# Performance work log

Hardware: AMD Instinct MI355X
Metric: run time of the kernel (lower is better)

The kernel has to match this reference:

```python
import jax, jax.numpy as jnp
import numpy as np

N_NODES = 100000
N_EDGES = 3200000
N_GRAPHS = 128
IN_DIM = 4
HID = 64
BN_EPS = 1e-5


def setup_inputs() -> dict:
    key = jax.random.key(0)
    ks = jax.random.split(key, 24)
    x = jax.random.normal(ks[0], (N_NODES, IN_DIM), dtype=jnp.float32)
    edge_index = jax.random.randint(ks[1], (2, N_EDGES), 0, N_NODES, dtype=jnp.int32)
    batch_ids = jnp.sort(jax.random.randint(ks[2], (N_NODES,), 0, N_GRAPHS, dtype=jnp.int32))

    def lin(k, out_d, in_d):
        s = 1.0 / np.sqrt(in_d)
        return jax.random.uniform(k, (out_d, in_d), jnp.float32, -s, s)

    inp = {
        'x': x, 'edge_index': edge_index, 'batch_ids': batch_ids,
        # SAGEConv i: out = lin_l(mean_neighbors) + lin_r(x_self); bias lives in lin_l
        'w1l': lin(ks[3], HID, IN_DIM), 'b1': jnp.zeros((HID,), jnp.float32), 'w1r': lin(ks[4], HID, IN_DIM),
        'bn1_g': jnp.ones((HID,), jnp.float32), 'bn1_b': jnp.zeros((HID,), jnp.float32),
        'w2l': lin(ks[5], HID, HID), 'b2': jnp.zeros((HID,), jnp.float32), 'w2r': lin(ks[6], HID, HID),
        'bn2_g': jnp.ones((HID,), jnp.float32), 'bn2_b': jnp.zeros((HID,), jnp.float32),
        'w3l': lin(ks[7], HID, HID), 'b3': jnp.zeros((HID,), jnp.float32), 'w3r': lin(ks[8], HID, HID),
        'bn3_g': jnp.ones((HID,), jnp.float32), 'bn3_b': jnp.zeros((HID,), jnp.float32),
        'fc1_w': lin(ks[9], 64, HID), 'fc1_b': jnp.zeros((64,), jnp.float32),
        'fc2_w': lin(ks[10], 2, 64), 'fc2_b': jnp.zeros((2,), jnp.float32),
    }
    return inp


def _sage(x, src, dst, deg_inv, wl, bl, wr):
    # mean-aggregate neighbor messages (source -> target), then two small GEMMs
    msum = jax.ops.segment_sum(x[src], dst, num_segments=N_NODES)  # [N, d]
    agg = msum * deg_inv[:, None]
    return agg @ wl.T + bl + x @ wr.T


def _bn(x, g, b):
    # BatchNorm1d in training mode: batch stats over node dim, biased variance
    m = jnp.mean(x, axis=0)
    v = jnp.mean((x - m) ** 2, axis=0)
    return (x - m) * jax.lax.rsqrt(v + BN_EPS) * g + b


def reference(x, edge_index, batch_ids,
              w1l, b1, w1r, bn1_g, bn1_b,
              w2l, b2, w2r, bn2_g, bn2_b,
              w3l, b3, w3r, bn3_g, bn3_b,
              fc1_w, fc1_b, fc2_w, fc2_b):
    src, dst = edge_index[0], edge_index[1]
    deg = jax.ops.segment_sum(jnp.ones((src.shape[0],), x.dtype), dst, num_segments=N_NODES)
    deg_inv = 1.0 / jnp.maximum(deg, 1.0)

    h = jax.nn.relu(_bn(_sage(x, src, dst, deg_inv, w1l, b1, w1r), bn1_g, bn1_b))
    h = jax.nn.relu(_bn(_sage(h, src, dst, deg_inv, w2l, b2, w2r), bn2_g, bn2_b))
    h = jax.nn.relu(_bn(_sage(h, src, dst, deg_inv, w3l, b3, w3r), bn3_g, bn3_b))

    # global_mean_pool over graphs
    gsum = jax.ops.segment_sum(h, batch_ids, num_segments=N_GRAPHS)
    gcnt = jax.ops.segment_sum(jnp.ones((h.shape[0],), h.dtype), batch_ids, num_segments=N_GRAPHS)
    pooled = gsum / jnp.maximum(gcnt, 1.0)[:, None]

    # MLP head (dropout = identity at inference)
    hid = jax.nn.relu(pooled @ fc1_w.T + fc1_b)
    return hid @ fc2_w.T + fc2_b
```

## Files before the change

kernel.cpp:

```cpp
#include <hip/hip_runtime.h>
#include <hip/hip_fp16.h>

#define NN 100000
#define NE 3200000
#define NG 128
#define BN_EPS 1e-5f

#define NBUK 782
#define BSHIFT 7
#define BCAP 6144

#define GRID_SG 1024
#define PBMAX 2048

typedef _Float16 h2v __attribute__((ext_vector_type(2)));

__global__ void __launch_bounds__(512) k_scatter(
    const int* __restrict__ src, const int* __restrict__ dst,
    int* __restrict__ slab_cursor, unsigned int* __restrict__ slab, int E) {
    __shared__ int hist[NBUK + 2];
    __shared__ int cbase[NBUK + 2];
    int tid = threadIdx.x;
    int eBeg = blockIdx.x * 6250;
    int eEnd = min(eBeg + 6250, E);

    for (int t = tid; t < NBUK; t += 512) hist[t] = 0;
    __syncthreads();
    for (int e = eBeg + tid; e < eEnd; e += 512) {
        int b = dst[e] >> BSHIFT;
        atomicAdd(&hist[b], 1);
    }
    __syncthreads();
    for (int t = tid; t < NBUK; t += 512) {
        int c = hist[t];
        cbase[t] = (c > 0) ? atomicAdd(&slab_cursor[t], c) : 0;
    }
    __syncthreads();
    for (int t = tid; t < NBUK; t += 512) hist[t] = 0;
    __syncthreads();
    for (int e = eBeg + tid; e < eEnd; e += 512) {
        int d = dst[e];
        int b = d >> BSHIFT;
        int r = atomicAdd(&hist[b], 1);
        int pos = cbase[b] + r;
        if (pos < BCAP) slab[(size_t)b * BCAP + pos] = ((unsigned)src[e] << BSHIFT) | (unsigned)(d & 127);
    }
}

__global__ void k_bucket_scan(const int* __restrict__ slab_cursor,
                              int* __restrict__ bucket_base, int* __restrict__ row_ptr) {
    __shared__ int sm[1024];
    int t = threadIdx.x;
    int c = (t < NBUK) ? min(slab_cursor[t], BCAP) : 0;
    sm[t] = c;
    __syncthreads();
    for (int off = 1; off < 1024; off <<= 1) {
        int add = (t >= off) ? sm[t - off] : 0;
        __syncthreads();
        sm[t] += add;
        __syncthreads();
    }
    if (t < NBUK) {
        bucket_base[t] = sm[t] - c;
        if (t == NBUK - 1) row_ptr[NN] = sm[t];
    }
}

__global__ void __launch_bounds__(512) k_bucket_csr(
    const unsigned int* __restrict__ slab, const int* __restrict__ slab_cursor,
    const int* __restrict__ bucket_base, int* __restrict__ row_ptr,
    float* __restrict__ deg_inv, int* __restrict__ csr_src,
    const float* __restrict__ x, const float* __restrict__ w1l,
    const float* __restrict__ b1, const float* __restrict__ w1r,
    float* __restrict__ h_pre, float* __restrict__ part) {
    __shared__ int lds_csr[BCAP];
    __shared__ int sdeg[128];
    __shared__ int sscan[128];
    __shared__ int slcur[128];
    __shared__ float swl[256], swr[256], sb1[64];
    __shared__ float ssum[64], ssq[64];
    int tid = threadIdx.x;
    int b = blockIdx.x;
    int lo = b << BSHIFT;
    int cnt = min(slab_cursor[b], BCAP);
    const unsigned int* sl = slab + (size_t)b * BCAP;

    if (tid < 256) { swl[tid] = w1l[tid]; swr[tid] = w1r[tid]; }
    if (tid < 64)  { sb1[tid] = b1[tid]; ssum[tid] = 0.f; ssq[tid] = 0.f; }
    if (tid < 128) sdeg[tid] = 0;
    __syncthreads();
    for (int k = tid; k < cnt; k += 512) {
        atomicAdd(&sdeg[sl[k] & 127], 1);
    }
    __syncthreads();
    int v = (tid < 128) ? sdeg[tid] : 0;
    if (tid < 128) sscan[tid] = v;
    __syncthreads();
    for (int off = 1; off < 128; off <<= 1) {
        int add = 0;
        if (tid < 128 && tid >= off) add = sscan[tid - off];
        __syncthreads();
        if (tid < 128) sscan[tid] += add;
        __syncthreads();
    }
    int base = bucket_base[b];
    if (tid < 128) {
        int excl = sscan[tid] - v;
        int n = lo + tid;
        if (n < NN) {
            row_ptr[n] = base + excl;
            deg_inv[n] = 1.0f / fmaxf((float)v, 1.0f);
        }
        slcur[tid] = excl;
    }
    __syncthreads();
    for (int k = tid; k < cnt; k += 512) {
        unsigned int p = sl[k];
        int pos = atomicAdd(&slcur[p & 127], 1);
        lds_csr[pos] = (int)(p >> BSHIFT);
    }
    __syncthreads();
    for (int k = tid; k < cnt; k += 512) csr_src[base + k] = lds_csr[k];

    int i = tid >> 2, c = tid & 3;
    int n = lo + i;
    bool valid = (n < NN);
    int dhi = sscan[i];
    int dlo = dhi - sdeg[i];
    const float4* x4 = (const float4*)x;
    float4 acc = make_float4(0.f, 0.f, 0.f, 0.f);
    for (int k = dlo + c; k < dhi; k += 4) {
        int s = lds_csr[k];
        float4 xv = x4[s];
        acc.x += xv.x; acc.y += xv.y; acc.z += xv.z; acc.w += xv.w;
    }
#pragma unroll
    for (int m = 1; m <= 2; m <<= 1) {
        acc.x += __shfl_xor(acc.x, m);
        acc.y += __shfl_xor(acc.y, m);
        acc.z += __shfl_xor(acc.z, m);
        acc.w += __shfl_xor(acc.w, m);
    }
    float dv = 1.0f / fmaxf((float)sdeg[i], 1.0f);
    float ax = acc.x * dv, ay = acc.y * dv, az = acc.z * dv, aw = acc.w * dv;
    float4 xs = valid ? x4[n] : make_float4(0.f, 0.f, 0.f, 0.f);

#pragma unroll
    for (int m4 = 0; m4 < 4; m4++) {
        float4 o = make_float4(0.f, 0.f, 0.f, 0.f);
        float* op = &o.x;
        if (valid) {
#pragma unroll
            for (int t = 0; t < 4; t++) {
                int j = c * 16 + m4 * 4 + t;
                float s = sb1[j];
                s += ax * swl[j * 4 + 0] + ay * swl[j * 4 + 1] + az * swl[j * 4 + 2] + aw * swl[j * 4 + 3];
                s += xs.x * swr[j * 4 + 0] + xs.y * swr[j * 4 + 1] + xs.z * swr[j * 4 + 2] + xs.w * swr[j * 4 + 3];
                op[t] = s;
            }
            ((float4*)h_pre)[(size_t)n * 16 + c * 4 + m4] = o;
        }
        float4 q = make_float4(o.x * o.x, o.y * o.y, o.z * o.z, o.w * o.w);
#pragma unroll
        for (int m = 4; m <= 32; m <<= 1) {
            o.x += __shfl_xor(o.x, m); o.y += __shfl_xor(o.y, m);
            o.z += __shfl_xor(o.z, m); o.w += __shfl_xor(o.w, m);
            q.x += __shfl_xor(q.x, m); q.y += __shfl_xor(q.y, m);
            q.z += __shfl_xor(q.z, m); q.w += __shfl_xor(q.w, m);
        }
        if ((tid & 63) < 4) {
            int jb = c * 16 + m4 * 4;
            atomicAdd(&ssum[jb + 0], o.x); atomicAdd(&ssum[jb + 1], o.y);
            atomicAdd(&ssum[jb + 2], o.z); atomicAdd(&ssum[jb + 3], o.w);
            atomicAdd(&ssq[jb + 0], q.x);  atomicAdd(&ssq[jb + 1], q.y);
            atomicAdd(&ssq[jb + 2], q.z);  atomicAdd(&ssq[jb + 3], q.w);
        }
    }
    __syncthreads();
    if (tid < 64) {
        part[(2 * tid) * PBMAX + blockIdx.x]     = ssum[tid];
        part[(2 * tid + 1) * PBMAX + blockIdx.x] = ssq[tid];
    }
}

__global__ void __launch_bounds__(512, 8) k_sage(
    const __half* __restrict__ h_in, const int* __restrict__ row_ptr,
    const int* __restrict__ csr_src, const float* __restrict__ deg_inv,
    const float* __restrict__ wl, const float* __restrict__ bl,
    const float* __restrict__ wr, float* __restrict__ h_pre,
    float* __restrict__ part) {
    __shared__ h2v wl2s[32][68];
    __shared__ h2v wr2s[32][68];
    __shared__ h2v tAh[32][36];
    __shared__ h2v tXh[32][36];
    __shared__ float ssum[64], ssq[64];
    int tid = threadIdx.x;
    for (int idx = tid; idx < 2048; idx += 512) {
        int j = idx & 63, kk = idx >> 6;
        float2 l = ((const float2*)wl)[j * 32 + kk];
        float2 r = ((const float2*)wr)[j * 32 + kk];
        wl2s[kk][j] = h2v{(_Float16)l.x, (_Float16)l.y};
        wr2s[kk][j] = h2v{(_Float16)r.x, (_Float16)r.y};
    }
    if (tid < 64) { ssum[tid] = 0.f; ssq[tid] = 0.f; }
    __syncthreads();

    int g = tid & 15, ni = tid >> 4;
    const uint2* tbl = (const uint2*)h_in;
    const int ntiles = NN / 32;

    for (int tile = blockIdx.x; tile < ntiles; tile += gridDim.x) {
        int n = tile * 32 + ni;
        float ax = 0.f, ay = 0.f, az = 0.f, aw = 0.f;
        int r0 = row_ptr[n], r1 = row_ptr[n + 1];
        int e = r0;
        for (; e + 8 <= r1; e += 8) {
            int s0 = csr_src[e],     s1 = csr_src[e + 1], s2 = csr_src[e + 2], s3 = csr_src[e + 3];
            int s4 = csr_src[e + 4], s5 = csr_src[e + 5], s6 = csr_src[e + 6], s7 = csr_src[e + 7];
            uint2 v0 = tbl[(size_t)s0 * 16 + g];
            uint2 v1 = tbl[(size_t)s1 * 16 + g];
            uint2 v2 = tbl[(size_t)s2 * 16 + g];
            uint2 v3 = tbl[(size_t)s3 * 16 + g];
            uint2 v4 = tbl[(size_t)s4 * 16 + g];
            uint2 v5 = tbl[(size_t)s5 * 16 + g];
            uint2 v6 = tbl[(size_t)s6 * 16 + g];
            uint2 v7 = tbl[(size_t)s7 * 16 + g];
            float2 f;
            f = __half22float2(*(__half2*)&v0.x); ax += f.x; ay += f.y;
            f = __half22float2(*(__half2*)&v0.y); az += f.x; aw += f.y;
            f = __half22float2(*(__half2*)&v1.x); ax += f.x; ay += f.y;
            f = __half22float2(*(__half2*)&v1.y); az += f.x; aw += f.y;
            f = __half22float2(*(__half2*)&v2.x); ax += f.x; ay += f.y;
            f = __half22float2(*(__half2*)&v2.y); az += f.x; aw += f.y;
            f = __half22float2(*(__half2*)&v3.x); ax += f.x; ay += f.y;
            f = __half22float2(*(__half2*)&v3.y); az += f.x; aw += f.y;
            f = __half22float2(*(__half2*)&v4.x); ax += f.x; ay += f.y;
            f = __half22float2(*(__half2*)&v4.y); az += f.x; aw += f.y;
            f = __half22float2(*(__half2*)&v5.x); ax += f.x; ay += f.y;
            f = __half22float2(*(__half2*)&v5.y); az += f.x; aw += f.y;
            f = __half22float2(*(__half2*)&v6.x); ax += f.x; ay += f.y;
            f = __half22float2(*(__half2*)&v6.y); az += f.x; aw += f.y;
            f = __half22float2(*(__half2*)&v7.x); ax += f.x; ay += f.y;
            f = __half22float2(*(__half2*)&v7.y); az += f.x; aw += f.y;
        }
        for (; e < r1; ++e) {
            int s = csr_src[e];
            uint2 v = tbl[(size_t)s * 16 + g];
            float2 f;
            f = __half22float2(*(__half2*)&v.x); ax += f.x; ay += f.y;
            f = __half22float2(*(__half2*)&v.y); az += f.x; aw += f.y;
        }
        float di = deg_inv[n];
        uint2 rs = tbl[(size_t)n * 16 + g];
        ax *= di; ay *= di; az *= di; aw *= di;
        tAh[ni][2 * g]     = h2v{(_Float16)ax, (_Float16)ay};
        tAh[ni][2 * g + 1] = h2v{(_Float16)az, (_Float16)aw};
        *(uint2*)&tXh[ni][2 * g] = rs;
        __syncthreads();

        float4 o = ((const float4*)bl)[g];
#pragma unroll 4
        for (int kk = 0; kk < 32; kk++) {
            h2v a2 = tAh[ni][kk];
            h2v x2 = tXh[ni][kk];
            h2v l0 = wl2s[kk][4 * g + 0], l1 = wl2s[kk][4 * g + 1];
            h2v l2 = wl2s[kk][4 * g + 2], l3 = wl2s[kk][4 * g + 3];
            h2v r0v = wr2s[kk][4 * g + 0], r1v = wr2s[kk][4 * g + 1];
            h2v r2v = wr2s[kk][4 * g + 2], r3v = wr2s[kk][4 * g + 3];
#if __has_builtin(__builtin_amdgcn_fdot2)
            o.x = __builtin_amdgcn_fdot2(a2, l0, o.x, false);
            o.y = __builtin_amdgcn_fdot2(a2, l1, o.y, false);
            o.z = __builtin_amdgcn_fdot2(a2, l2, o.z, false);
            o.w = __builtin_amdgcn_fdot2(a2, l3, o.w, false);
            o.x = __builtin_amdgcn_fdot2(x2, r0v, o.x, false);
            o.y = __builtin_amdgcn_fdot2(x2, r1v, o.y, false);
            o.z = __builtin_amdgcn_fdot2(x2, r2v, o.z, false);
            o.w = __builtin_amdgcn_fdot2(x2, r3v, o.w, false);
#else
            float b0 = (float)a2.x, b1 = (float)a2.y, x0 = (float)x2.x, x1 = (float)x2.y;
            o.x += b0 * (float)l0.x + b1 * (float)l0.y + x0 * (float)r0v.x + x1 * (float)r0v.y;
            o.y += b0 * (float)l1.x + b1 * (float)l1.y + x0 * (float)r1v.x + x1 * (float)r1v.y;
            o.z += b0 * (float)l2.x + b1 * (float)l2.y + x0 * (float)r2v.x + x1 * (float)r2v.y;
            o.w += b0 * (float)l3.x + b1 * (float)l3.y + x0 * (float)r3v.x + x1 * (float)r3v.y;
#endif
        }
        ((float4*)h_pre)[(size_t)n * 16 + g] = o;

        float4 qv = make_float4(o.x * o.x, o.y * o.y, o.z * o.z, o.w * o.w);
#pragma unroll
        for (int m = 16; m <= 32; m <<= 1) {
            o.x += __shfl_xor(o.x, m); o.y += __shfl_xor(o.y, m);
            o.z += __shfl_xor(o.z, m); o.w += __shfl_xor(o.w, m);
            qv.x += __shfl_xor(qv.x, m); qv.y += __shfl_xor(qv.y, m);
            qv.z += __shfl_xor(qv.z, m); qv.w += __shfl_xor(qv.w, m);
        }
        if ((tid & 48) == 0) {
            atomicAdd(&ssum[4 * g + 0], o.x); atomicAdd(&ssum[4 * g + 1], o.y);
            atomicAdd(&ssum[4 * g + 2], o.z); atomicAdd(&ssum[4 * g + 3], o.w);
            atomicAdd(&ssq[4 * g + 0], qv.x);  atomicAdd(&ssq[4 * g + 1], qv.y);
            atomicAdd(&ssq[4 * g + 2], qv.z);  atomicAdd(&ssq[4 * g + 3], qv.w);
        }
        __syncthreads();
    }
    if (tid < 64) {
        part[(2 * tid) * PBMAX + blockIdx.x]     = ssum[tid];
        part[(2 * tid + 1) * PBMAX + blockIdx.x] = ssq[tid];
    }
}

__global__ void k_reduce_sb(const float* __restrict__ part, int PB,
                            const float* __restrict__ gamma, const float* __restrict__ beta,
                            float* __restrict__ sbv, int N) {
    int c = blockIdx.x;
    float s = 0.f, q = 0.f;
    for (int b = threadIdx.x; b < PB; b += 256) {
        s += part[(2 * c) * PBMAX + b];
        q += part[(2 * c + 1) * PBMAX + b];
    }
    __shared__ float rs[256], rq[256];
    rs[threadIdx.x] = s;
    rq[threadIdx.x] = q;
    __syncthreads();
    for (int off = 128; off > 0; off >>= 1) {
        if (threadIdx.x < off) {
            rs[threadIdx.x] += rs[threadIdx.x + off];
            rq[threadIdx.x] += rq[threadIdx.x + off];
        }
        __syncthreads();
    }
    if (threadIdx.x == 0) {
        float m = rs[0] / (float)N;
        float var = rq[0] / (float)N - m * m;
        float sc = gamma[c] * rsqrtf(var + BN_EPS);
        sbv[c]      = sc;
        sbv[64 + c] = beta[c] - m * sc;
    }
}

__global__ void k_bnrelu_h(const float* __restrict__ h_pre, const float* __restrict__ sbv,
                           __half* __restrict__ h, int N) {
    __shared__ float s_sc[64], s_bi[64];
    if (threadIdx.x < 64) {
        s_sc[threadIdx.x] = sbv[threadIdx.x];
        s_bi[threadIdx.x] = sbv[64 + threadIdx.x];
    }
    __syncthreads();
    int total = N * 16;
    for (int i = blockIdx.x * blockDim.x + threadIdx.x; i < total; i += gridDim.x * blockDim.x) {
        float4 v = ((const float4*)h_pre)[i];
        int c4 = (i & 15) * 4;
        v.x = fmaxf(v.x * s_sc[c4 + 0] + s_bi[c4 + 0], 0.f);
        v.y = fmaxf(v.y * s_sc[c4 + 1] + s_bi[c4 + 1], 0.f);
        v.z = fmaxf(v.z * s_sc[c4 + 2] + s_bi[c4 + 2], 0.f);
        v.w = fmaxf(v.w * s_sc[c4 + 3] + s_bi[c4 + 3], 0.f);
        __half2 p0 = __floats2half2_rn(v.x, v.y);
        __half2 p1 = __floats2half2_rn(v.z, v.w);
        uint2 o;
        o.x = *(unsigned int*)&p0;
        o.y = *(unsigned int*)&p1;
        ((uint2*)h)[i] = o;
    }
}

__global__ void k_poolhead(const __half* __restrict__ h, const int* __restrict__ batch,
                           const float* __restrict__ fc1w, const float* __restrict__ fc1b,
                           const float* __restrict__ fc2w, const float* __restrict__ fc2b,
                           float* __restrict__ out, int N) {
    int gph = blockIdx.x;
    int lo = 0, hi = N;
    while (lo < hi) { int mid = (lo + hi) >> 1; if (batch[mid] < gph) lo = mid + 1; else hi = mid; }
    int start = lo;
    hi = N;
    while (lo < hi) { int mid = (lo + hi) >> 1; if (batch[mid] < gph + 1) lo = mid + 1; else hi = mid; }
    int end = lo;

    int c = threadIdx.x & 63, w = threadIdx.x >> 6;
    float s = 0.f;
    for (int r = start + w; r < end; r += 4) s += __half2float(h[(size_t)r * 64 + c]);
    __shared__ float sm[256];
    __shared__ float pl[64], hid[64];
    sm[threadIdx.x] = s;
    __syncthreads();
    if (threadIdx.x < 64) {
        float t = sm[c] + sm[64 + c] + sm[128 + c] + sm[192 + c];
        pl[c] = t / fmaxf((float)(end - start), 1.0f);
    }
    __syncthreads();
    if (threadIdx.x < 64) {
        int j = threadIdx.x;
        float v = fc1b[j];
        for (int k = 0; k < 64; k++) v += pl[k] * fc1w[j * 64 + k];
        hid[j] = fmaxf(v, 0.f);
    }
    __syncthreads();
    if (threadIdx.x < 2) {
        int j = threadIdx.x;
        float o = fc2b[j];
        for (int k = 0; k < 64; k++) o += hid[k] * fc2w[j * 64 + k];
        out[gph * 2 + j] = o;
    }
}

extern "C" void kernel_launch(void* const* d_in, const int* in_sizes, int n_in,
                              void* d_out, int out_size, void* d_ws, size_t ws_size,
                              hipStream_t stream) {
    const float* x    = (const float*)d_in[0];
    const int* ei     = (const int*)d_in[1];
    const int* batch  = (const int*)d_in[2];
    const float* w1l  = (const float*)d_in[3];
    const float* b1   = (const float*)d_in[4];
    const float* w1r  = (const float*)d_in[5];
    const float* bn1g = (const float*)d_in[6];
    const float* bn1b = (const float*)d_in[7];
    const float* w2l  = (const float*)d_in[8];
    const float* b2   = (const float*)d_in[9];
    const float* w2r  = (const float*)d_in[10];
    const float* bn2g = (const float*)d_in[11];
    const float* bn2b = (const float*)d_in[12];
    const float* w3l  = (const float*)d_in[13];
    const float* b3   = (const float*)d_in[14];
    const float* w3r  = (const float*)d_in[15];
    const float* bn3g = (const float*)d_in[16];
    const float* bn3b = (const float*)d_in[17];
    const float* fc1w = (const float*)d_in[18];
    const float* fc1b = (const float*)d_in[19];
    const float* fc2w = (const float*)d_in[20];
    const float* fc2b = (const float*)d_in[21];
    float* out = (float*)d_out;

    const int N = NN, E = NE;
    const int* srcp = ei;
    const int* dstp = ei + E;

    char* ws = (char*)d_ws;
    size_t off = 0;
    auto alloc = [&](size_t bytes) -> char* {
        char* p = ws + off;
        off += (bytes + 255) & ~(size_t)255;
        return p;
    };
    int* csr_src       = (int*)alloc(sizeof(int) * E);
    float* hB          = (float*)alloc(sizeof(float) * N * 64);
    __half* hH         = (__half*)alloc(sizeof(__half) * N * 64);
    unsigned int* slab = (unsigned int*)alloc(sizeof(unsigned int) * (size_t)NBUK * BCAP);
    int* slab_cursor   = (int*)alloc(sizeof(int) * NBUK);
    int* bucket_base   = (int*)alloc(sizeof(int) * NBUK);
    int* row_ptr       = (int*)alloc(sizeof(int) * (N + 1));
    float* deg_inv     = (float*)alloc(sizeof(float) * N);
    float* part        = (float*)alloc(sizeof(float) * 128 * PBMAX);
    float* sbv         = (float*)alloc(sizeof(float) * 128);

    hipMemsetAsync(slab_cursor, 0, sizeof(int) * NBUK, stream);

    k_scatter<<<512, 512, 0, stream>>>(srcp, dstp, slab_cursor, slab, E);
    k_bucket_scan<<<1, 1024, 0, stream>>>(slab_cursor, bucket_base, row_ptr);
    k_bucket_csr<<<NBUK, 512, 0, stream>>>(slab, slab_cursor, bucket_base, row_ptr, deg_inv,
                                           csr_src, x, w1l, b1, w1r, hB, part);
    k_reduce_sb<<<64, 256, 0, stream>>>(part, NBUK, bn1g, bn1b, sbv, N);
    k_bnrelu_h<<<1024, 256, 0, stream>>>(hB, sbv, hH, N);

    k_sage<<<GRID_SG, 512, 0, stream>>>(hH, row_ptr, csr_src, deg_inv, w2l, b2, w2r, hB, part);
    k_reduce_sb<<<64, 256, 0, stream>>>(part, GRID_SG, bn2g, bn2b, sbv, N);
    k_bnrelu_h<<<1024, 256, 0, stream>>>(hB, sbv, hH, N);

    k_sage<<<GRID_SG, 512, 0, stream>>>(hH, row_ptr, csr_src, deg_inv, w3l, b3, w3r, hB, part);
    k_reduce_sb<<<64, 256, 0, stream>>>(part, GRID_SG, bn3g, bn3b, sbv, N);
    k_bnrelu_h<<<1024, 256, 0, stream>>>(hB, sbv, hH, N);

    k_poolhead<<<NG, 256, 0, stream>>>(hH, batch, fc1w, fc1b, fc2w, fc2b, out, N);
}
```

Measured before the change: 447.7 us.

## Fold BN stat reduction into producer kernels via last-block pattern; fuse final BN into pool

```diff
diff --git a/kernel.cpp b/kernel.cpp
--- a/kernel.cpp
+++ b/kernel.cpp
@@ -66,19 +66,56 @@
     }
 }
 
+__device__ inline void lastblock_reduce(float* __restrict__ part, int PB,
+                                        const float* __restrict__ gamma,
+                                        const float* __restrict__ beta,
+                                        float* __restrict__ sbv, int* __restrict__ counter,
+                                        int grid_n, float* rs, float* rq, int* amLast) {
+    int tid = threadIdx.x;
+    __threadfence();
+    if (tid == 0) {
+        int old = __hip_atomic_fetch_add(counter, 1, __ATOMIC_ACQ_REL, __HIP_MEMORY_SCOPE_AGENT);
+        *amLast = (old == grid_n - 1);
+    }
+    __syncthreads();
+    if (!*amLast) return;
+    int c = tid & 63, w = tid >> 6;
+    float s = 0.f, q = 0.f;
+    for (int b = w; b < PB; b += 8) {
+        s += __hip_atomic_load(&part[(2 * c) * PBMAX + b], __ATOMIC_RELAXED, __HIP_MEMORY_SCOPE_AGENT);
+        q += __hip_atomic_load(&part[(2 * c + 1) * PBMAX + b], __ATOMIC_RELAXED, __HIP_MEMORY_SCOPE_AGENT);
+    }
+    rs[tid] = s; rq[tid] = q;
+    __syncthreads();
+    if (tid < 64) {
+        float ts = 0.f, tq = 0.f;
+#pragma unroll
+        for (int k = 0; k < 8; k++) { ts += rs[k * 64 + c]; tq += rq[k * 64 + c]; }
+        float m = ts / (float)NN;
+        float var = tq / (float)NN - m * m;
+        float sc = gamma[c] * rsqrtf(var + BN_EPS);
+        sbv[c]      = sc;
+        sbv[64 + c] = beta[c] - m * sc;
+    }
+}
+
 __global__ void __launch_bounds__(512) k_bucket_csr(
     const unsigned int* __restrict__ slab, const int* __restrict__ slab_cursor,
     const int* __restrict__ bucket_base, int* __restrict__ row_ptr,
     float* __restrict__ deg_inv, int* __restrict__ csr_src,
     const float* __restrict__ x, const float* __restrict__ w1l,
     const float* __restrict__ b1, const float* __restrict__ w1r,
-    float* __restrict__ h_pre, float* __restrict__ part) {
+    float* __restrict__ h_pre, float* __restrict__ part,
+    const float* __restrict__ gamma, const float* __restrict__ beta,
+    float* __restrict__ sbv, int* __restrict__ counter) {
     __shared__ int lds_csr[BCAP];
     __shared__ int sdeg[128];
     __shared__ int sscan[128];
     __shared__ int slcur[128];
     __shared__ float swl[256], swr[256], sb1[64];
     __shared__ float ssum[64], ssq[64];
+    __shared__ float rs[512], rq[512];
+    __shared__ int amLast;
     int tid = threadIdx.x;
     int b = blockIdx.x;
     int lo = b << BSHIFT;
@@ -181,6 +218,7 @@
         part[(2 * tid) * PBMAX + blockIdx.x]     = ssum[tid];
         part[(2 * tid + 1) * PBMAX + blockIdx.x] = ssq[tid];
     }
+    lastblock_reduce(part, NBUK, gamma, beta, sbv, counter, NBUK, rs, rq, &amLast);
 }
 
 __global__ void __launch_bounds__(512, 8) k_sage(
@@ -188,12 +226,16 @@
     const int* __restrict__ csr_src, const float* __restrict__ deg_inv,
     const float* __restrict__ wl, const float* __restrict__ bl,
     const float* __restrict__ wr, float* __restrict__ h_pre,
-    float* __restrict__ part) {
+    float* __restrict__ part,
+    const float* __restrict__ gamma, const float* __restrict__ beta,
+    float* __restrict__ sbv, int* __restrict__ counter) {
     __shared__ h2v wl2s[32][68];
     __shared__ h2v wr2s[32][68];
     __shared__ h2v tAh[32][36];
     __shared__ h2v tXh[32][36];
     __shared__ float ssum[64], ssq[64];
+    __shared__ float rs[512], rq[512];
+    __shared__ int amLast;
     int tid = threadIdx.x;
     for (int idx = tid; idx < 2048; idx += 512) {
         int j = idx & 63, kk = idx >> 6;
@@ -209,7 +251,7 @@
     const uint2* tbl = (const uint2*)h_in;
     const int ntiles = NN / 32;
 
-    for (int tile = blockIdx.x; tile < ntiles; tile += gridDim.x) {
+    for (int tile = blockIdx.x; tile < ntiles; tile += GRID_SG) {
         int n = tile * 32 + ni;
         float ax = 0.f, ay = 0.f, az = 0.f, aw = 0.f;
         int r0 = row_ptr[n], r1 = row_ptr[n + 1];
@@ -251,11 +293,11 @@
             f = __half22float2(*(__half2*)&v.y); az += f.x; aw += f.y;
         }
         float di = deg_inv[n];
-        uint2 rs = tbl[(size_t)n * 16 + g];
+        uint2 rsv = tbl[(size_t)n * 16 + g];
         ax *= di; ay *= di; az *= di; aw *= di;
         tAh[ni][2 * g]     = h2v{(_Float16)ax, (_Float16)ay};
         tAh[ni][2 * g + 1] = h2v{(_Float16)az, (_Float16)aw};
-        *(uint2*)&tXh[ni][2 * g] = rs;
+        *(uint2*)&tXh[ni][2 * g] = rsv;
         __syncthreads();
 
         float4 o = ((const float4*)bl)[g];
@@ -306,35 +348,7 @@
         part[(2 * tid) * PBMAX + blockIdx.x]     = ssum[tid];
         part[(2 * tid + 1) * PBMAX + blockIdx.x] = ssq[tid];
     }
-}
-
-__global__ void k_reduce_sb(const float* __restrict__ part, int PB,
-                            const float* __restrict__ gamma, const float* __restrict__ beta,
-                            float* __restrict__ sbv, int N) {
-    int c = blockIdx.x;
-    float s = 0.f, q = 0.f;
-    for (int b = threadIdx.x; b < PB; b += 256) {
-        s += part[(2 * c) * PBMAX + b];
-        q += part[(2 * c + 1) * PBMAX + b];
-    }
-    __shared__ float rs[256], rq[256];
-    rs[threadIdx.x] = s;
-    rq[threadIdx.x] = q;
-    __syncthreads();
-    for (int off = 128; off > 0; off >>= 1) {
-        if (threadIdx.x < off) {
-            rs[threadIdx.x] += rs[threadIdx.x + off];
-            rq[threadIdx.x] += rq[threadIdx.x + off];
-        }
-        __syncthreads();
-    }
-    if (threadIdx.x == 0) {
-        float m = rs[0] / (float)N;
-        float var = rq[0] / (float)N - m * m;
-        float sc = gamma[c] * rsqrtf(var + BN_EPS);
-        sbv[c]      = sc;
-        sbv[64 + c] = beta[c] - m * sc;
-    }
+    lastblock_reduce(part, GRID_SG, gamma, beta, sbv, counter, GRID_SG, rs, rq, &amLast);
 }
 
 __global__ void k_bnrelu_h(const float* __restrict__ h_pre, const float* __restrict__ sbv,
@@ -362,10 +376,19 @@
     }
 }
 
-__global__ void k_poolhead(const __half* __restrict__ h, const int* __restrict__ batch,
+__global__ void k_poolhead(const float* __restrict__ hB, const float* __restrict__ sbv,
+                           const int* __restrict__ batch,
                            const float* __restrict__ fc1w, const float* __restrict__ fc1b,
                            const float* __restrict__ fc2w, const float* __restrict__ fc2b,
                            float* __restrict__ out, int N) {
+    __shared__ float ssc[64], sbi[64];
+    __shared__ float sm[256];
+    __shared__ float pl[64], hid[64];
+    if (threadIdx.x < 64) {
+        ssc[threadIdx.x] = sbv[threadIdx.x];
+        sbi[threadIdx.x] = sbv[64 + threadIdx.x];
+    }
+    __syncthreads();
     int gph = blockIdx.x;
     int lo = 0, hi = N;
     while (lo < hi) { int mid = (lo + hi) >> 1; if (batch[mid] < gph) lo = mid + 1; else hi = mid; }
@@ -376,9 +399,8 @@
 
     int c = threadIdx.x & 63, w = threadIdx.x >> 6;
     float s = 0.f;
-    for (int r = start + w; r < end; r += 4) s += __half2float(h[(size_t)r * 64 + c]);
-    __shared__ float sm[256];
-    __shared__ float pl[64], hid[64];
+    for (int r = start + w; r < end; r += 4)
+        s += fmaxf(hB[(size_t)r * 64 + c] * ssc[c] + sbi[c], 0.f);
     sm[threadIdx.x] = s;
     __syncthreads();
     if (threadIdx.x < 64) {
@@ -443,29 +465,28 @@
     float* hB          = (float*)alloc(sizeof(float) * N * 64);
     __half* hH         = (__half*)alloc(sizeof(__half) * N * 64);
     unsigned int* slab = (unsigned int*)alloc(sizeof(unsigned int) * (size_t)NBUK * BCAP);
-    int* slab_cursor   = (int*)alloc(sizeof(int) * NBUK);
+    int* slab_cursor   = (int*)alloc(sizeof(int) * (NBUK + 16));
+    int* counters      = slab_cursor + NBUK;
     int* bucket_base   = (int*)alloc(sizeof(int) * NBUK);
     int* row_ptr       = (int*)alloc(sizeof(int) * (N + 1));
     float* deg_inv     = (float*)alloc(sizeof(float) * N);
     float* part        = (float*)alloc(sizeof(float) * 128 * PBMAX);
     float* sbv         = (float*)alloc(sizeof(float) * 128);
 
-    hipMemsetAsync(slab_cursor, 0, sizeof(int) * NBUK, stream);
+    hipMemsetAsync(slab_cursor, 0, sizeof(int) * (NBUK + 16), stream);
 
     k_scatter<<<512, 512, 0, stream>>>(srcp, dstp, slab_cursor, slab, E);
     k_bucket_scan<<<1, 1024, 0, stream>>>(slab_cursor, bucket_base, row_ptr);
     k_bucket_csr<<<NBUK, 512, 0, stream>>>(slab, slab_cursor, bucket_base, row_ptr, deg_inv,
-                                           csr_src, x, w1l, b1, w1r, hB, part);
-    k_reduce_sb<<<64, 256, 0, stream>>>(part, NBUK, bn1g, bn1b, sbv, N);
+                                           csr_src, x, w1l, b1, w1r, hB, part,
+                                           bn1g, bn1b, sbv, &counters[0]);
     k_bnrelu_h<<<1024, 256, 0, stream>>>(hB, sbv, hH, N);
 
-    k_sage<<<GRID_SG, 512, 0, stream>>>(hH, row_ptr, csr_src, deg_inv, w2l, b2, w2r, hB, part);
-    k_reduce_sb<<<64, 256, 0, stream>>>(part, GRID_SG, bn2g, bn2b, sbv, N);
+    k_sage<<<GRID_SG, 512, 0, stream>>>(hH, row_ptr, csr_src, deg_inv, w2l, b2, w2r, hB, part,
+                                        bn2g, bn2b, sbv, &counters[1]);
     k_bnrelu_h<<<1024, 256, 0, stream>>>(hB, sbv, hH, N);
 
-    k_sage<<<GRID_SG, 512, 0, stream>>>(hH, row_ptr, csr_src, deg_inv, w3l, b3, w3r, hB, part);
-    k_reduce_sb<<<64, 256, 0, stream>>>(part, GRID_SG, bn3g, bn3b, sbv, N);
-    k_bnrelu_h<<<1024, 256, 0, stream>>>(hB, sbv, hH, N);
-
-    k_poolhead<<<NG, 256, 0, stream>>>(hH, batch, fc1w, fc1b, fc2w, fc2b, out, N);
-}
+    k_sage<<<GRID_SG, 512, 0, stream>>>(hH, row_ptr, csr_src, deg_inv, w3l, b3, w3r, hB, part,
+                                        bn3g, bn3b, sbv, &counters[2]);
+    k_poolhead<<<NG, 256, 0, stream>>>(hB, sbv, batch, fc1w, fc1b, fc2w, fc2b, out, N);
+}
```

Result: slower. 1.301 ms (+190.7%).
